# Kernel optimization log

Measured on AMD Instinct MI355X. Metric: run time of the kernel, lower is better.

## Reference

```python
import jax, jax.numpy as jnp
import numpy as np

NUM_CLASSES = 19
IGNORE = 255
KLD_MARGIN = 3.0
DEC = 0.01
BOT_EPS, TOP_EPS = 1e-4, 1.0
# eight-corner neighbor offsets (size=1), order matches AAF layers.eightcorner_activation
EDGE_OFFS = ((-1, -1), (-1, 0), (-1, 1), (0, -1), (0, 1), (1, -1), (1, 0), (1, 1))


def _shift(x, dy, dx, pad_val):
    # Shift along H,W (axes 1,2): out[:, y, x] = x[:, y+dy, x+dx], padded with pad_val.
    pads = [(0, 0), (1, 1), (1, 1)] + [(0, 0)] * (x.ndim - 3)
    xp = jnp.pad(x, pads, constant_values=pad_val)
    h, w = x.shape[1], x.shape[2]
    return xp[:, 1 + dy:1 + dy + h, 1 + dx:1 + dx + w]


def _resize_bilinear_ac(x, oh, ow):
    # torch F.interpolate(mode='bilinear', align_corners=True) on NCHW.
    n, c, h, w = x.shape
    ys = jnp.linspace(0.0, h - 1.0, oh)
    xs = jnp.linspace(0.0, w - 1.0, ow)
    y0 = jnp.floor(ys).astype(jnp.int32); y1 = jnp.minimum(y0 + 1, h - 1)
    x0 = jnp.floor(xs).astype(jnp.int32); x1 = jnp.minimum(x0 + 1, w - 1)
    wy = (ys - y0).astype(x.dtype)[None, None, :, None]
    wx = (xs - x0).astype(x.dtype)[None, None, None, :]
    rows = x[:, :, y0, :] * (1.0 - wy) + x[:, :, y1, :] * wy  # (N,C,oh,W)
    return rows[:, :, :, x0] * (1.0 - wx) + rows[:, :, :, x1] * wx  # (N,C,oh,ow)


def setup_inputs() -> dict:
    key = jax.random.key(0)
    k1, k2 = jax.random.split(key)
    preds = jax.random.normal(k1, (2, NUM_CLASSES, 64, 64), dtype=jnp.float32)
    targets = jax.random.randint(k2, (2, 512, 512), 0, NUM_CLASSES, dtype=jnp.int32)
    w_edge = jnp.zeros((1, 1, 1, NUM_CLASSES, 1, 3), dtype=jnp.float32)
    w_not_edge = jnp.zeros((1, 1, 1, NUM_CLASSES, 1, 3), dtype=jnp.float32)
    return {"preds": preds, "targets": targets, "w_edge": w_edge, "w_not_edge": w_not_edge}


def reference(preds, targets, w_edge, w_not_edge):
    h, w = targets.shape[1], targets.shape[2]
    pred = _resize_bilinear_ac(preds, h, w)          # (N,C,H,W)
    prob = jax.nn.softmax(pred, axis=1)
    prob = jnp.transpose(prob, (0, 2, 3, 1))          # (N,H,W,C) NHWC layout used by AAF layers

    labels = targets                                  # (N,H,W)
    ign = labels == IGNORE
    one_label = jnp.where(ign, 0, labels)
    ohl = jax.nn.one_hot(one_label, NUM_CLASSES, dtype=jnp.float32)  # (N,H,W,C)
    ohl = jnp.where(ign[..., None], float(IGNORE), ohl)

    # edge/non-edge class weights: softmax over last dim, take index 0 -> (1,1,1,C,1)
    w_e = jax.nn.softmax(w_edge, axis=-1)[..., 0]
    w_ne = jax.nn.softmax(w_not_edge, axis=-1)[..., 0]

    # ignores_from_label: bidirectional ignore mask, neighbor order is reversed offsets
    ignore_c = labels > NUM_CLASSES - 1               # (N,H,W)
    ignore8 = jnp.stack([_shift(ignore_c, -dy, -dx, True) | ignore_c for dy, dx in EDGE_OFFS], axis=-1)
    not_ignore = ~ignore8[:, :, :, None, :]           # (N,H,W,1,8)

    # edges_from_label: neighbor label (padded with ignore_class) differs from center
    edge8 = jnp.stack([_shift(ohl, dy, dx, float(IGNORE)) != ohl for dy, dx in EDGE_OFFS], axis=-1)  # (N,H,W,C,8)
    edge = edge8 & not_ignore
    not_edge = (~edge) & not_ignore

    # eightcorner_activation on probabilities (zero padded)
    probs_paired = jnp.stack([_shift(prob, dy, dx, 0.0) for dy, dx in EDGE_OFFS], axis=-1)  # (N,H,W,C,8)
    p = prob[..., None]                               # (N,H,W,C,1)
    pc = jnp.clip(p, BOT_EPS, TOP_EPS)
    npc = jnp.clip(1.0 - p, BOT_EPS, TOP_EPS)
    ppc = jnp.clip(probs_paired, BOT_EPS, TOP_EPS)
    nppc = jnp.clip(1.0 - probs_paired, BOT_EPS, TOP_EPS)

    # binary KL divergence per class/neighbor
    kldiv = ppc * jnp.log(ppc / pc) + nppc * jnp.log(nppc / npc)  # (N,H,W,C,8)

    # per-pixel class weights: sum_c w[c]*one_hot[c] -> (N,H,W,1,1)
    we_map = jnp.sum(w_e * ohl[..., None], axis=3, keepdims=True)
    wne_map = jnp.sum(w_ne * ohl[..., None], axis=3, keepdims=True)

    edge_loss = jnp.maximum(0.0, KLD_MARGIN - kldiv) * we_map
    not_edge_loss = kldiv * wne_map

    # torch.mean over gathered nonzero indices == masked sum / count
    e_cnt = jnp.maximum(jnp.sum(edge), 1).astype(jnp.float32)
    ne_cnt = jnp.maximum(jnp.sum(not_edge), 1).astype(jnp.float32)
    e_mean = jnp.sum(jnp.where(edge, edge_loss, 0.0)) / e_cnt
    ne_mean = jnp.sum(jnp.where(not_edge, not_edge_loss, 0.0)) / ne_cnt

    return e_mean * 1.0 * DEC + ne_mean * 1.0 * DEC
```

## Files before the change

### kernel.cpp

```cpp
#include <hip/hip_runtime.h>
#include <stdint.h>


#define NC 19
#define HH 512
#define WW 512
#define NB 2
#define TS 16
#define HS 18
#define HP (HS * HS)
#define ATRS 20
#define PS 25
#define NBLK 2048
#define LOG2E 1.4426950408889634f
#define LN2 0.6931471805599453f
#define LOG2EPS -13.287712379549449f
#define K2F 4.3280851226668906f
#define K2PAD 4.328125f

typedef _Float16 f16x2 __attribute__((ext_vector_type(2)));

#if __has_builtin(__builtin_amdgcn_exp2f)
#define EXP2F(x) __builtin_amdgcn_exp2f(x)
#else
#define EXP2F(x) __expf((x) * LN2)
#endif

#if __has_builtin(__builtin_amdgcn_fdot2)
#define FDOT2(a, b, c) __builtin_amdgcn_fdot2((a), (b), (c), false)
#else
#define FDOT2(a, b, c) fmaf((float)(a)[1], (float)(b)[1], fmaf((float)(a)[0], (float)(b)[0], (c)))
#endif

struct Part { float es, ns; unsigned int cnt, pad; };

union U32F2 { uint32_t u; f16x2 h; };
__device__ __forceinline__ uint32_t bc_u32(f16x2 v) { U32F2 x; x.h = v; return x.u; }
__device__ __forceinline__ f16x2 bc_h2(uint32_t v) { U32F2 x; x.u = v; return x.h; }
__device__ __forceinline__ float extf(f16x2 v, int h) { return h ? (float)v[1] : (float)v[0]; }

template <bool KEEP>
__device__ __forceinline__ int pix_compute(const float* __restrict__ patch,
                                           const int* __restrict__ tg,
                                           int y, int x, int y0b, int x0b,
                                           uint32_t* __restrict__ ATrow,
                                           f16x2* Dh, f16x2* Lh) {
    const bool oob = ((unsigned)y >= (unsigned)HH) | ((unsigned)x >= (unsigned)WW);
    if (oob) {
        const _Float16 aP = (_Float16)1e-4f, dP = (_Float16)LOG2EPS;
        const _Float16 tP = (_Float16)((float)aP * (float)dP);
        const uint32_t aPP = bc_u32((f16x2){aP, aP});
        const uint32_t tPP = bc_u32((f16x2){tP, tP});
        const uint32_t aPL = bc_u32((f16x2){aP, (_Float16)0.0f});
        const uint32_t tPL = bc_u32((f16x2){tP, (_Float16)0.0f});
#pragma unroll
        for (int i = 0; i < 5; ++i) {
            uint4 wv;
            wv.x = aPP; wv.y = tPP;
            wv.z = (i < 4) ? aPP : aPL;
            wv.w = (i < 4) ? tPP : tPL;
            *reinterpret_cast<uint4*>(ATrow + 4 * i) = wv;
            if (KEEP) {
                Dh[2 * i] = (f16x2){dP, dP};
                Dh[2 * i + 1] = (i < 4) ? (f16x2){dP, dP} : (f16x2){dP, (_Float16)0.0f};
                Lh[2 * i] = (f16x2){(_Float16)0.0f, (_Float16)0.0f};
                Lh[2 * i + 1] = (f16x2){(_Float16)0.0f, (_Float16)0.0f};
            }
        }
        return 255;
    }

    const int lab = tg[(y << 9) + x];
    const float fy = (float)(y * 63) / 511.0f;
    const float fx = (float)(x * 63) / 511.0f;
    const int y0 = (int)fy, x0 = (int)fx;
    const float wy = fy - (float)y0, wx = fx - (float)x0;
    const int y1 = min(y0 + 1, 63), x1 = min(x0 + 1, 63);
    const float omwy = 1.0f - wy, omwx = 1.0f - wx;
    const float w00 = omwy * omwx, w01 = omwy * wx;
    const float w10 = wy * omwx,   w11 = wy * wx;
    const int o00 = (y0 - y0b) * 5 + (x0 - x0b);
    const int o01 = o00 + (x1 - x0);
    const int o10 = o00 + (y1 - y0) * 5;
    const int o11 = o10 + (x1 - x0);

    float v2[NC], w[NC];
    float s = 0.0f;
#pragma unroll
    for (int c = 0; c < NC; ++c) {
        const float* pc_ = &patch[c * PS];
        const float vv = fmaf(pc_[o00], w00, fmaf(pc_[o01], w01,
                          fmaf(pc_[o10], w10, pc_[o11] * w11)));
        v2[c] = vv;
        const float e = EXP2F(vv);
        w[c] = e;
        s += e;
    }
    const float inv = 1.0f / s;
    const float lns2 = __log2f(s);

#pragma unroll
    for (int i = 0; i < 5; ++i) {
        _Float16 av[4], tv[4], dv[4], lv[4];
#pragma unroll
        for (int q = 0; q < 4; ++q) {
            const int c = 4 * i + q;
            _Float16 a16 = (_Float16)0.0f, d16 = (_Float16)0.0f,
                     l16 = (_Float16)0.0f, t16 = (_Float16)0.0f;
            if (c < NC) {
                const float p = w[c] * inv;
                const float la = fmaxf(v2[c] - lns2, LOG2EPS);
                const float aa = fmaxf(p, 1e-4f);
                const float lb = __log2f(fmaxf(1.0f - p, 1e-4f));
                a16 = (_Float16)aa;
                d16 = (_Float16)(la - lb);
                l16 = (_Float16)lb;
                t16 = a16 * d16 + l16;
            }
            av[q] = a16; tv[q] = t16; dv[q] = d16; lv[q] = l16;
        }
        uint4 wv;
        wv.x = bc_u32((f16x2){av[0], av[1]});
        wv.y = bc_u32((f16x2){tv[0], tv[1]});
        wv.z = bc_u32((f16x2){av[2], av[3]});
        wv.w = bc_u32((f16x2){tv[2], tv[3]});
        *reinterpret_cast<uint4*>(ATrow + 4 * i) = wv;
        if (KEEP) {
            Dh[2 * i] = (f16x2){dv[0], dv[1]};
            Dh[2 * i + 1] = (f16x2){dv[2], dv[3]};
            Lh[2 * i] = (f16x2){lv[0], lv[1]};
            Lh[2 * i + 1] = (f16x2){lv[2], lv[3]};
        }
    }
    return lab;
}

__global__ __launch_bounds__(256, 5) void k_fused(const float* __restrict__ preds,
                                                  const int* __restrict__ targets,
                                                  const float* __restrict__ w_edge,
                                                  const float* __restrict__ w_not_edge,
                                                  Part* __restrict__ pb) {
    __shared__ __align__(16) uint32_t AT[HP * ATRS];
    __shared__ int   TG[HP];
    __shared__ float swe[NC], swn[NC];
    __shared__ float patch[NC * PS];
    __shared__ float r_es[4], r_ns[4];
    __shared__ unsigned int r_cnt[4];

    const int tid = threadIdx.x;
    const int bx = blockIdx.x, by = blockIdx.y, n = blockIdx.z;

    if (tid < NC) {
        {
            float a = w_edge[tid * 3 + 0], b = w_edge[tid * 3 + 1], c = w_edge[tid * 3 + 2];
            float m = fmaxf(a, fmaxf(b, c));
            float ea = __expf(a - m), eb = __expf(b - m), ec = __expf(c - m);
            swe[tid] = (ea / (ea + eb + ec)) * LN2;
        }
        {
            float a = w_not_edge[tid * 3 + 0], b = w_not_edge[tid * 3 + 1], c = w_not_edge[tid * 3 + 2];
            float m = fmaxf(a, fmaxf(b, c));
            float ea = __expf(a - m), eb = __expf(b - m), ec = __expf(c - m);
            swn[tid] = (ea / (ea + eb + ec)) * LN2;
        }
    }

    const int* tg = targets + (n << 18);
    const float* pbase = preds + (size_t)n * NC * 4096;

    const int ty = tid >> 4, tx = tid & 15;
    const int hi = (ty + 1) * HS + (tx + 1);
    const int DOFF[8] = {-HS - 1, -HS, -HS + 1, -1, 1, HS - 1, HS, HS + 1};
    const f16x2 one2 = {(_Float16)1.0f, (_Float16)1.0f};
    const f16x2 k32 = {(_Float16)K2F, (_Float16)K2F};
    const f16x2 z2 = {(_Float16)0.0f, (_Float16)0.0f};

    float e_s = 0.0f, ne_s = 0.0f;
    unsigned int cnt = 0;

    const int yT = max(by * TS - 1, 0), xL = max(bx * TS - 1, 0);
    const int y0b = (yT * 63) / 511, x0b = (xL * 63) / 511;
    for (int t = tid; t < NC * PS; t += 256) {
        const int c = t / PS, r = t - c * PS;
        const int ry = r / 5, rx = r - ry * 5;
        const int sy = min(y0b + ry, 63), sx = min(x0b + rx, 63);
        patch[t] = pbase[c * 4096 + (sy << 6) + sx] * LOG2E;
    }
    __syncthreads();

    if (tid < 68) {
        int i;
        if (tid < 18)      i = tid;
        else if (tid < 36) i = 306 + (tid - 18);
        else if (tid < 52) i = (tid - 35) * HS;
        else               i = (tid - 51) * HS + 17;
        const int hy = i / HS, hx = i - hy * HS;
        TG[i] = pix_compute<false>(patch, tg, by * TS + hy - 1, bx * TS + hx - 1,
                                   y0b, x0b, &AT[i * ATRS], nullptr, nullptr);
    }

    f16x2 Dh[10], Lh[10];
    const int lab = pix_compute<true>(patch, tg, by * TS + ty, bx * TS + tx,
                                      y0b, x0b, &AT[hi * ATRS], Dh, Lh);
    TG[hi] = lab;
    __syncthreads();

    const bool interior_blk = (bx > 0) & (bx < 31) & (by > 0) & (by < 31);
    const int plab = lab >> 1, hlab = lab & 1;
    float es_h = 0.0f, ns_h = 0.0f;
    unsigned int cnt_h = 0;

    if (interior_blk) {
#pragma unroll
        for (int k = 0; k < 8; ++k) {
            const int np = hi + DOFF[k];
            const int nlab = TG[np];
            const int pn = nlab >> 1, hn = nlab & 1;
            const uint32_t* wbp = &AT[np * ATRS];
            float dot0 = 0.0f, dot1 = 0.0f;
            f16x2 klLw = z2, klNw = z2;
#pragma unroll
            for (int i = 0; i < 5; ++i) {
                const uint4 rd = *reinterpret_cast<const uint4*>(wbp + 4 * i);
                const int j0 = 2 * i, j1 = 2 * i + 1;
                const f16x2 kl20 = bc_h2(rd.y) - (bc_h2(rd.x) * Dh[j0] + Lh[j0]);
                const f16x2 kl21 = bc_h2(rd.w) - (bc_h2(rd.z) * Dh[j1] + Lh[j1]);
                dot0 = FDOT2(kl20, one2, dot0);
                dot1 = FDOT2(kl21, one2, dot1);
                klLw = (j0 == plab) ? kl20 : klLw;
                klLw = (j1 == plab) ? kl21 : klLw;
                klNw = (j0 == pn) ? kl20 : klNw;
                klNw = (j1 == pn) ? kl21 : klNw;
            }
            const float dot = dot0 + dot1;
            const float klL = extf(klLw, hlab);
            const float klN = extf(klNw, hn);
            const bool df = (lab != nlab);
            const float w = df ? 1.0f : 0.0f;
            es_h = fmaf(w, fmaxf(K2F - klL, 0.0f) + fmaxf(K2F - klN, 0.0f), es_h);
            ns_h += dot - w * (klL + klN);
            cnt_h += df ? ((2u << 16) | (NC - 2)) : NC;
        }
        e_s = fmaf(es_h, swe[lab], e_s);
        ne_s = fmaf(ns_h, swn[lab], ne_s);
        cnt += cnt_h;
    } else if (lab <= NC - 1) {
#pragma unroll
        for (int k = 0; k < 8; ++k) {
            const int off = DOFF[k];
            const int rlab = TG[hi - off];
            const int np = hi + off;
            const int nlab = TG[np];
            const int pn = nlab >> 1, hn = nlab & 1;
            const uint32_t* wbp = &AT[np * ATRS];
            float dot0 = 0.0f, dot1 = 0.0f, ekall = 0.0f;
            f16x2 klLw = z2, klNw = z2;
#pragma unroll
            for (int i = 0; i < 5; ++i) {
                const uint4 rd = *reinterpret_cast<const uint4*>(wbp + 4 * i);
                const int j0 = 2 * i, j1 = 2 * i + 1;
                const f16x2 kl20 = bc_h2(rd.y) - (bc_h2(rd.x) * Dh[j0] + Lh[j0]);
                const f16x2 kl21 = bc_h2(rd.w) - (bc_h2(rd.z) * Dh[j1] + Lh[j1]);
                dot0 = FDOT2(kl20, one2, dot0);
                dot1 = FDOT2(kl21, one2, dot1);
                f16x2 m0 = k32 - kl20, m1 = k32 - kl21;
                m0[0] = m0[0] > (_Float16)0.0f ? m0[0] : (_Float16)0.0f;
                m0[1] = m0[1] > (_Float16)0.0f ? m0[1] : (_Float16)0.0f;
                m1[0] = m1[0] > (_Float16)0.0f ? m1[0] : (_Float16)0.0f;
                m1[1] = m1[1] > (_Float16)0.0f ? m1[1] : (_Float16)0.0f;
                ekall = FDOT2(m0, one2, ekall);
                ekall = FDOT2(m1, one2, ekall);
                klLw = (j0 == plab) ? kl20 : klLw;
                klLw = (j1 == plab) ? kl21 : klLw;
                klNw = (j0 == pn) ? kl20 : klNw;
                klNw = (j1 == pn) ? kl21 : klNw;
            }
            const float dot = dot0 + dot1;
            const float klL = extf(klLw, hlab);
            const float klN = extf(klNw, hn);
            const bool isPad = (nlab == 255);
            const bool df = (lab != nlab) && !isPad;
            const float w = df ? 1.0f : 0.0f;
            const float ek_int = w * (fmaxf(K2F - klL, 0.0f) + fmaxf(K2F - klN, 0.0f));
            const float nk_int = dot - w * (klL + klN);
            const float ek_pad = ekall - K2PAD;
            const float ek_k = isPad ? ek_pad : ek_int;
            const float nk_k = isPad ? 0.0f : nk_int;
            const unsigned int pc = isPad ? NC : (df ? 2u : 0u);
            const bool valid = (rlab <= NC - 1);
            const float vf = valid ? 1.0f : 0.0f;
            es_h = fmaf(vf, ek_k, es_h);
            ns_h = fmaf(vf, nk_k, ns_h);
            cnt_h += valid ? ((pc << 16) | (NC - pc)) : 0u;
        }
        e_s = fmaf(es_h, swe[lab], e_s);
        ne_s = fmaf(ns_h, swn[lab], ne_s);
        cnt += cnt_h;
    }

#pragma unroll
    for (int off = 32; off > 0; off >>= 1) {
        e_s  += __shfl_down(e_s, off, 64);
        ne_s += __shfl_down(ne_s, off, 64);
        cnt  += __shfl_down(cnt, off, 64);
    }
    const int wid = tid >> 6, lane = tid & 63;
    if (lane == 0) { r_es[wid] = e_s; r_ns[wid] = ne_s; r_cnt[wid] = cnt; }
    __syncthreads();
    if (tid == 0) {
        float tes = 0.0f, tns = 0.0f;
        unsigned int tc = 0;
#pragma unroll
        for (int w = 0; w < 4; ++w) { tes += r_es[w]; tns += r_ns[w]; tc += r_cnt[w]; }
        const int bid = (blockIdx.z * gridDim.y + blockIdx.y) * gridDim.x + blockIdx.x;
        pb[bid].es = tes; pb[bid].ns = tns; pb[bid].cnt = tc; pb[bid].pad = 0;
    }
}

__global__ __launch_bounds__(256) void k_final(const Part* __restrict__ pb,
                                               float* __restrict__ out) {
    const int tid = threadIdx.x;
    double es = 0.0, ns = 0.0;
    long long ec = 0, nc = 0;
    for (int i = tid; i < NBLK; i += 256) {
        es += (double)pb[i].es; ns += (double)pb[i].ns;
        const unsigned int c = pb[i].cnt;
        ec += (long long)(c >> 16); nc += (long long)(c & 0xFFFFu);
    }
#pragma unroll
    for (int off = 32; off > 0; off >>= 1) {
        es += __shfl_down(es, off, 64);
        ns += __shfl_down(ns, off, 64);
        ec += __shfl_down(ec, off, 64);
        nc += __shfl_down(nc, off, 64);
    }
    __shared__ double ses[4], sns[4];
    __shared__ long long sec[4], snc[4];
    const int wid = tid >> 6, lane = tid & 63;
    if (lane == 0) { ses[wid] = es; sns[wid] = ns; sec[wid] = ec; snc[wid] = nc; }
    __syncthreads();
    if (tid == 0) {
        double tes = 0.0, tns = 0.0;
        long long tec = 0, tnc = 0;
#pragma unroll
        for (int w = 0; w < 4; ++w) { tes += ses[w]; tns += sns[w]; tec += sec[w]; tnc += snc[w]; }
        double ecd = (double)tec; if (ecd < 1.0) ecd = 1.0;
        double ncd = (double)tnc; if (ncd < 1.0) ncd = 1.0;
        out[0] = (float)((tes / ecd) * 0.01 + (tns / ncd) * 0.01);
    }
}

extern "C" void kernel_launch(void* const* d_in, const int* in_sizes, int n_in,
                              void* d_out, int out_size, void* d_ws, size_t ws_size,
                              hipStream_t stream) {
    const float* preds      = (const float*)d_in[0];
    const int*   targets    = (const int*)d_in[1];
    const float* w_edge     = (const float*)d_in[2];
    const float* w_not_edge = (const float*)d_in[3];

    Part* pb = (Part*)d_ws;

    dim3 grid(WW / TS, HH / TS, NB);
    k_fused<<<grid, 256, 0, stream>>>(preds, targets, w_edge, w_not_edge, pb);
    k_final<<<1, 256, 0, stream>>>(pb, (float*)d_out);
}
```

Before: 88.74 us.

## Use taller 32x16 tiles with 512-thread blocks to cut halo overhead

Doubles the tile height to 32 rows with 512 threads per block, so the halo ring is recomputed for a smaller share of pixels and half as many blocks write partials. The label tile moves to bytes and the per-block counts are split into separate edge and not-edge fields to avoid 16-bit packing overflow with more pixels. In exchange, shared memory per block and register pressure under the new launch bounds rise, which may reduce occupancy. The patch size grows to 35 values per class, apparently to cover the taller source footprint.

```diff
diff --git a/kernel.cpp b/kernel.cpp
--- a/kernel.cpp
+++ b/kernel.cpp
@@ -6,12 +6,14 @@
 #define HH 512
 #define WW 512
 #define NB 2
-#define TS 16
+#define TSY 32
+#define TSX 16
 #define HS 18
-#define HP (HS * HS)
+#define VS 34
+#define HP (VS * HS)
 #define ATRS 20
-#define PS 25
-#define NBLK 2048
+#define PS 35
+#define NBLK 1024
 #define LOG2E 1.4426950408889634f
 #define LN2 0.6931471805599453f
 #define LOG2EPS -13.287712379549449f
@@ -32,7 +34,7 @@
 #define FDOT2(a, b, c) fmaf((float)(a)[1], (float)(b)[1], fmaf((float)(a)[0], (float)(b)[0], (c)))
 #endif
 
-struct Part { float es, ns; unsigned int cnt, pad; };
+struct Part { float es, ns; unsigned int ec, nc; };
 
 union U32F2 { uint32_t u; f16x2 h; };
 __device__ __forceinline__ uint32_t bc_u32(f16x2 v) { U32F2 x; x.h = v; return x.u; }
@@ -135,17 +137,17 @@
     return lab;
 }
 
-__global__ __launch_bounds__(256, 5) void k_fused(const float* __restrict__ preds,
+__global__ __launch_bounds__(512, 6) void k_fused(const float* __restrict__ preds,
                                                   const int* __restrict__ targets,
                                                   const float* __restrict__ w_edge,
                                                   const float* __restrict__ w_not_edge,
                                                   Part* __restrict__ pb) {
     __shared__ __align__(16) uint32_t AT[HP * ATRS];
-    __shared__ int   TG[HP];
+    __shared__ uint8_t TG[HP];
     __shared__ float swe[NC], swn[NC];
     __shared__ float patch[NC * PS];
-    __shared__ float r_es[4], r_ns[4];
-    __shared__ unsigned int r_cnt[4];
+    __shared__ float r_es[8], r_ns[8];
+    __shared__ unsigned int r_cnt[8];
 
     const int tid = threadIdx.x;
     const int bx = blockIdx.x, by = blockIdx.y, n = blockIdx.z;
@@ -178,9 +180,9 @@
     float e_s = 0.0f, ne_s = 0.0f;
     unsigned int cnt = 0;
 
-    const int yT = max(by * TS - 1, 0), xL = max(bx * TS - 1, 0);
+    const int yT = max(by * TSY - 1, 0), xL = max(bx * TSX - 1, 0);
     const int y0b = (yT * 63) / 511, x0b = (xL * 63) / 511;
-    for (int t = tid; t < NC * PS; t += 256) {
+    for (int t = tid; t < NC * PS; t += 512) {
         const int c = t / PS, r = t - c * PS;
         const int ry = r / 5, rx = r - ry * 5;
         const int sy = min(y0b + ry, 63), sx = min(x0b + rx, 63);
@@ -188,24 +190,24 @@
     }
     __syncthreads();
 
-    if (tid < 68) {
+    if (tid < 100) {
         int i;
         if (tid < 18)      i = tid;
-        else if (tid < 36) i = 306 + (tid - 18);
-        else if (tid < 52) i = (tid - 35) * HS;
-        else               i = (tid - 51) * HS + 17;
+        else if (tid < 36) i = 33 * HS + (tid - 18);
+        else if (tid < 68) i = (tid - 35) * HS;
+        else               i = (tid - 67) * HS + 17;
         const int hy = i / HS, hx = i - hy * HS;
-        TG[i] = pix_compute<false>(patch, tg, by * TS + hy - 1, bx * TS + hx - 1,
-                                   y0b, x0b, &AT[i * ATRS], nullptr, nullptr);
+        TG[i] = (uint8_t)pix_compute<false>(patch, tg, by * TSY + hy - 1, bx * TSX + hx - 1,
+                                            y0b, x0b, &AT[i * ATRS], nullptr, nullptr);
     }
 
     f16x2 Dh[10], Lh[10];
-    const int lab = pix_compute<true>(patch, tg, by * TS + ty, bx * TS + tx,
+    const int lab = pix_compute<true>(patch, tg, by * TSY + ty, bx * TSX + tx,
                                       y0b, x0b, &AT[hi * ATRS], Dh, Lh);
-    TG[hi] = lab;
+    TG[hi] = (uint8_t)lab;
     __syncthreads();
 
-    const bool interior_blk = (bx > 0) & (bx < 31) & (by > 0) & (by < 31);
+    const bool interior_blk = (bx > 0) & (bx < 31) & (by > 0) & (by < 15);
     const int plab = lab >> 1, hlab = lab & 1;
     float es_h = 0.0f, ns_h = 0.0f;
     unsigned int cnt_h = 0;
@@ -214,7 +216,7 @@
 #pragma unroll
         for (int k = 0; k < 8; ++k) {
             const int np = hi + DOFF[k];
-            const int nlab = TG[np];
+            const int nlab = (int)TG[np];
             const int pn = nlab >> 1, hn = nlab & 1;
             const uint32_t* wbp = &AT[np * ATRS];
             float dot0 = 0.0f, dot1 = 0.0f;
@@ -248,9 +250,9 @@
 #pragma unroll
         for (int k = 0; k < 8; ++k) {
             const int off = DOFF[k];
-            const int rlab = TG[hi - off];
+            const int rlab = (int)TG[hi - off];
             const int np = hi + off;
-            const int nlab = TG[np];
+            const int nlab = (int)TG[np];
             const int pn = nlab >> 1, hn = nlab & 1;
             const uint32_t* wbp = &AT[np * ATRS];
             float dot0 = 0.0f, dot1 = 0.0f, ekall = 0.0f;
@@ -309,11 +311,14 @@
     __syncthreads();
     if (tid == 0) {
         float tes = 0.0f, tns = 0.0f;
-        unsigned int tc = 0;
-#pragma unroll
-        for (int w = 0; w < 4; ++w) { tes += r_es[w]; tns += r_ns[w]; tc += r_cnt[w]; }
+        unsigned int tec = 0, tnc = 0;
+#pragma unroll
+        for (int w = 0; w < 8; ++w) {
+            tes += r_es[w]; tns += r_ns[w];
+            tec += r_cnt[w] >> 16; tnc += r_cnt[w] & 0xFFFFu;
+        }
         const int bid = (blockIdx.z * gridDim.y + blockIdx.y) * gridDim.x + blockIdx.x;
-        pb[bid].es = tes; pb[bid].ns = tns; pb[bid].cnt = tc; pb[bid].pad = 0;
+        pb[bid].es = tes; pb[bid].ns = tns; pb[bid].ec = tec; pb[bid].nc = tnc;
     }
 }
 
@@ -324,8 +329,7 @@
     long long ec = 0, nc = 0;
     for (int i = tid; i < NBLK; i += 256) {
         es += (double)pb[i].es; ns += (double)pb[i].ns;
-        const unsigned int c = pb[i].cnt;
-        ec += (long long)(c >> 16); nc += (long long)(c & 0xFFFFu);
+        ec += (long long)pb[i].ec; nc += (long long)pb[i].nc;
     }
 #pragma unroll
     for (int off = 32; off > 0; off >>= 1) {
@@ -360,7 +364,7 @@
 
     Part* pb = (Part*)d_ws;
 
-    dim3 grid(WW / TS, HH / TS, NB);
-    k_fused<<<grid, 256, 0, stream>>>(preds, targets, w_edge, w_not_edge, pb);
+    dim3 grid(WW / TSX, HH / TSY, NB);
+    k_fused<<<grid, 512, 0, stream>>>(preds, targets, w_edge, w_not_edge, pb);
     k_final<<<1, 256, 0, stream>>>(pb, (float*)d_out);
 }
```

New measurement: 86.32 us (median of 2 runs). 2.7% less time.

## Algebraically reduce per-neighbor KL sums to dot products with precomputed pixel terms

Applied to the files above, without the earlier changes.

Rewrites the per-neighbor binary KL summation so that the sum over classes is a single packed fp16 dot product of the neighbor's clipped probabilities against the pixel's log-ratio vector, plus precomputed per-pixel scalars (T, SL). The label and class weight of each pixel are packed together into one shared word. Per-pixel label-specific terms are computed once. In deep interior blocks, the neighbor-label KL contribution is attributed symmetrically from the owning pixel's side, which avoids extra gathers. This cuts fp16 arithmetic per neighbor and restructures the LDS layout, at the cost of more code paths, extra log2 calls and changed rounding behaviour.

```diff
diff --git a/kernel.cpp b/kernel.cpp
--- a/kernel.cpp
+++ b/kernel.cpp
@@ -33,39 +33,55 @@
 #endif
 
 struct Part { float es, ns; unsigned int cnt, pad; };
+struct Own { float SL, u, v, dlab, llab; };
 
 union U32F2 { uint32_t u; f16x2 h; };
 __device__ __forceinline__ uint32_t bc_u32(f16x2 v) { U32F2 x; x.h = v; return x.u; }
 __device__ __forceinline__ f16x2 bc_h2(uint32_t v) { U32F2 x; x.u = v; return x.h; }
 __device__ __forceinline__ float extf(f16x2 v, int h) { return h ? (float)v[1] : (float)v[0]; }
+
+union U16H { uint16_t u; _Float16 h; };
+__device__ __forceinline__ uint32_t pack_TL(int lab, float T) {
+    U16H t; t.h = (_Float16)T;
+    return ((uint32_t)lab << 16) | (uint32_t)t.u;
+}
+__device__ __forceinline__ float TL_T(uint32_t tl) {
+    U16H t; t.u = (uint16_t)(tl & 0xFFFFu);
+    return (float)t.h;
+}
 
 template <bool KEEP>
 __device__ __forceinline__ int pix_compute(const float* __restrict__ patch,
                                            const int* __restrict__ tg,
                                            int y, int x, int y0b, int x0b,
                                            uint32_t* __restrict__ ATrow,
-                                           f16x2* Dh, f16x2* Lh) {
+                                           uint32_t* __restrict__ TLw,
+                                           f16x2* Dh, f16x2* Lh, Own* os) {
     const bool oob = ((unsigned)y >= (unsigned)HH) | ((unsigned)x >= (unsigned)WW);
     if (oob) {
-        const _Float16 aP = (_Float16)1e-4f, dP = (_Float16)LOG2EPS;
-        const _Float16 tP = (_Float16)((float)aP * (float)dP);
+        const _Float16 aP = (_Float16)1e-4f;
         const uint32_t aPP = bc_u32((f16x2){aP, aP});
-        const uint32_t tPP = bc_u32((f16x2){tP, tP});
         const uint32_t aPL = bc_u32((f16x2){aP, (_Float16)0.0f});
-        const uint32_t tPL = bc_u32((f16x2){tP, (_Float16)0.0f});
-#pragma unroll
-        for (int i = 0; i < 5; ++i) {
-            uint4 wv;
-            wv.x = aPP; wv.y = tPP;
-            wv.z = (i < 4) ? aPP : aPL;
-            wv.w = (i < 4) ? tPP : tPL;
-            *reinterpret_cast<uint4*>(ATrow + 4 * i) = wv;
-            if (KEEP) {
-                Dh[2 * i] = (f16x2){dP, dP};
-                Dh[2 * i + 1] = (i < 4) ? (f16x2){dP, dP} : (f16x2){dP, (_Float16)0.0f};
-                Lh[2 * i] = (f16x2){(_Float16)0.0f, (_Float16)0.0f};
-                Lh[2 * i + 1] = (f16x2){(_Float16)0.0f, (_Float16)0.0f};
+        uint4 W0, W1, W2, W3, W4;
+        W0.x = aPP; W0.y = aPP; W0.z = aPP; W0.w = aPP;
+        W1 = W0;
+        W2.x = aPP; W2.y = aPL; W2.z = 0u; W2.w = 0u;
+        W3.x = 0u; W3.y = 0u; W3.z = 0u; W3.w = 0u;
+        W4 = W3;
+        *reinterpret_cast<uint4*>(ATrow + 0)  = W0;
+        *reinterpret_cast<uint4*>(ATrow + 4)  = W1;
+        *reinterpret_cast<uint4*>(ATrow + 8)  = W2;
+        *reinterpret_cast<uint4*>(ATrow + 12) = W3;
+        *reinterpret_cast<uint4*>(ATrow + 16) = W4;
+        *TLw = pack_TL(255, 0.0f);
+        if (KEEP) {
+            const _Float16 dP = (_Float16)LOG2EPS;
+#pragma unroll
+            for (int j = 0; j < 10; ++j) {
+                Dh[j] = (j < 9) ? (f16x2){dP, dP} : (f16x2){dP, (_Float16)0.0f};
+                Lh[j] = (f16x2){(_Float16)0.0f, (_Float16)0.0f};
             }
+            os->SL = 0.0f; os->u = 0.0f; os->v = 0.0f; os->dlab = 0.0f; os->llab = 0.0f;
         }
         return 255;
     }
@@ -99,38 +115,65 @@
     const float inv = 1.0f / s;
     const float lns2 = __log2f(s);
 
-#pragma unroll
-    for (int i = 0; i < 5; ++i) {
-        _Float16 av[4], tv[4], dv[4], lv[4];
-#pragma unroll
-        for (int q = 0; q < 4; ++q) {
-            const int c = 4 * i + q;
-            _Float16 a16 = (_Float16)0.0f, d16 = (_Float16)0.0f,
-                     l16 = (_Float16)0.0f, t16 = (_Float16)0.0f;
-            if (c < NC) {
-                const float p = w[c] * inv;
-                const float la = fmaxf(v2[c] - lns2, LOG2EPS);
-                const float aa = fmaxf(p, 1e-4f);
-                const float lb = __log2f(fmaxf(1.0f - p, 1e-4f));
-                a16 = (_Float16)aa;
-                d16 = (_Float16)(la - lb);
-                l16 = (_Float16)lb;
-                t16 = a16 * d16 + l16;
-            }
-            av[q] = a16; tv[q] = t16; dv[q] = d16; lv[q] = l16;
-        }
-        uint4 wv;
-        wv.x = bc_u32((f16x2){av[0], av[1]});
-        wv.y = bc_u32((f16x2){tv[0], tv[1]});
-        wv.z = bc_u32((f16x2){av[2], av[3]});
-        wv.w = bc_u32((f16x2){tv[2], tv[3]});
-        *reinterpret_cast<uint4*>(ATrow + 4 * i) = wv;
-        if (KEEP) {
-            Dh[2 * i] = (f16x2){dv[0], dv[1]};
-            Dh[2 * i + 1] = (f16x2){dv[2], dv[3]};
-            Lh[2 * i] = (f16x2){lv[0], lv[1]};
-            Lh[2 * i + 1] = (f16x2){lv[2], lv[3]};
-        }
+    float Tdd = 0.0f, SL = 0.0f;
+    uint32_t aw_[10], lw_[10];
+#pragma unroll
+    for (int j = 0; j < 10; ++j) {
+        _Float16 a0 = (_Float16)0.0f, l0 = (_Float16)0.0f, d0 = (_Float16)0.0f;
+        _Float16 a1 = (_Float16)0.0f, l1 = (_Float16)0.0f, d1 = (_Float16)0.0f;
+        {
+            const int c = 2 * j;
+            const float p = w[c] * inv;
+            const float la = fmaxf(v2[c] - lns2, LOG2EPS);
+            const float aa = fmaxf(p, 1e-4f);
+            const float lb = __log2f(fmaxf(1.0f - p, 1e-4f));
+            const float dd = la - lb;
+            Tdd = fmaf(aa, dd, Tdd); SL += lb;
+            a0 = (_Float16)aa; l0 = (_Float16)lb; d0 = (_Float16)dd;
+        }
+        if (2 * j + 1 < NC) {
+            const int c = 2 * j + 1;
+            const float p = w[c] * inv;
+            const float la = fmaxf(v2[c] - lns2, LOG2EPS);
+            const float aa = fmaxf(p, 1e-4f);
+            const float lb = __log2f(fmaxf(1.0f - p, 1e-4f));
+            const float dd = la - lb;
+            Tdd = fmaf(aa, dd, Tdd); SL += lb;
+            a1 = (_Float16)aa; l1 = (_Float16)lb; d1 = (_Float16)dd;
+        }
+        aw_[j] = bc_u32((f16x2){a0, a1});
+        lw_[j] = bc_u32((f16x2){l0, l1});
+        if (KEEP) { Dh[j] = (f16x2){d0, d1}; Lh[j] = (f16x2){l0, l1}; }
+    }
+    {
+        uint4 W0, W1, W2, W3, W4;
+        W0.x = aw_[0]; W0.y = aw_[1]; W0.z = aw_[2]; W0.w = aw_[3];
+        W1.x = aw_[4]; W1.y = aw_[5]; W1.z = aw_[6]; W1.w = aw_[7];
+        W2.x = aw_[8]; W2.y = aw_[9]; W2.z = lw_[0]; W2.w = lw_[1];
+        W3.x = lw_[2]; W3.y = lw_[3]; W3.z = lw_[4]; W3.w = lw_[5];
+        W4.x = lw_[6]; W4.y = lw_[7]; W4.z = lw_[8]; W4.w = lw_[9];
+        *reinterpret_cast<uint4*>(ATrow + 0)  = W0;
+        *reinterpret_cast<uint4*>(ATrow + 4)  = W1;
+        *reinterpret_cast<uint4*>(ATrow + 8)  = W2;
+        *reinterpret_cast<uint4*>(ATrow + 12) = W3;
+        *reinterpret_cast<uint4*>(ATrow + 16) = W4;
+    }
+    *TLw = pack_TL(lab, Tdd + SL);
+
+    if (KEEP) {
+        const float* pl = &patch[lab * PS];
+        const float vlab = fmaf(pl[o00], w00, fmaf(pl[o01], w01,
+                            fmaf(pl[o10], w10, pl[o11] * w11)));
+        const float p = EXP2F(vlab) * inv;
+        const float la = fmaxf(vlab - lns2, LOG2EPS);
+        const float aa = fmaxf(p, 1e-4f);
+        const float lb = __log2f(fmaxf(1.0f - p, 1e-4f));
+        const float dd = la - lb;
+        os->SL = SL;
+        os->dlab = dd;
+        os->llab = lb;
+        os->u = fmaf(aa, dd, lb);
+        os->v = aa;
     }
     return lab;
 }
@@ -141,8 +184,8 @@
                                                   const float* __restrict__ w_not_edge,
                                                   Part* __restrict__ pb) {
     __shared__ __align__(16) uint32_t AT[HP * ATRS];
-    __shared__ int   TG[HP];
-    __shared__ float swe[NC], swn[NC];
+    __shared__ uint32_t TL[HP];
+    __shared__ float2 swen[NC];
     __shared__ float patch[NC * PS];
     __shared__ float r_es[4], r_ns[4];
     __shared__ unsigned int r_cnt[4];
@@ -151,18 +194,20 @@
     const int bx = blockIdx.x, by = blockIdx.y, n = blockIdx.z;
 
     if (tid < NC) {
+        float sw_e, sw_n;
         {
             float a = w_edge[tid * 3 + 0], b = w_edge[tid * 3 + 1], c = w_edge[tid * 3 + 2];
             float m = fmaxf(a, fmaxf(b, c));
             float ea = __expf(a - m), eb = __expf(b - m), ec = __expf(c - m);
-            swe[tid] = (ea / (ea + eb + ec)) * LN2;
+            sw_e = (ea / (ea + eb + ec)) * LN2;
         }
         {
             float a = w_not_edge[tid * 3 + 0], b = w_not_edge[tid * 3 + 1], c = w_not_edge[tid * 3 + 2];
             float m = fmaxf(a, fmaxf(b, c));
             float ea = __expf(a - m), eb = __expf(b - m), ec = __expf(c - m);
-            swn[tid] = (ea / (ea + eb + ec)) * LN2;
-        }
+            sw_n = (ea / (ea + eb + ec)) * LN2;
+        }
+        swen[tid] = make_float2(sw_e, sw_n);
     }
 
     const int* tg = targets + (n << 18);
@@ -171,9 +216,10 @@
     const int ty = tid >> 4, tx = tid & 15;
     const int hi = (ty + 1) * HS + (tx + 1);
     const int DOFF[8] = {-HS - 1, -HS, -HS + 1, -1, 1, HS - 1, HS, HS + 1};
+    const int DY[8] = {-1, -1, -1, 0, 0, 1, 1, 1};
+    const int DX[8] = {-1, 0, 1, -1, 1, -1, 0, 1};
     const f16x2 one2 = {(_Float16)1.0f, (_Float16)1.0f};
     const f16x2 k32 = {(_Float16)K2F, (_Float16)K2F};
-    const f16x2 z2 = {(_Float16)0.0f, (_Float16)0.0f};
 
     float e_s = 0.0f, ne_s = 0.0f;
     unsigned int cnt = 0;
@@ -195,107 +241,192 @@
         else if (tid < 52) i = (tid - 35) * HS;
         else               i = (tid - 51) * HS + 17;
         const int hy = i / HS, hx = i - hy * HS;
-        TG[i] = pix_compute<false>(patch, tg, by * TS + hy - 1, bx * TS + hx - 1,
-                                   y0b, x0b, &AT[i * ATRS], nullptr, nullptr);
+        pix_compute<false>(patch, tg, by * TS + hy - 1, bx * TS + hx - 1,
+                           y0b, x0b, &AT[i * ATRS], &TL[i], nullptr, nullptr, nullptr);
     }
 
     f16x2 Dh[10], Lh[10];
+    Own os;
     const int lab = pix_compute<true>(patch, tg, by * TS + ty, bx * TS + tx,
-                                      y0b, x0b, &AT[hi * ATRS], Dh, Lh);
-    TG[hi] = lab;
+                                      y0b, x0b, &AT[hi * ATRS], &TL[hi], Dh, Lh, &os);
     __syncthreads();
 
     const bool interior_blk = (bx > 0) & (bx < 31) & (by > 0) & (by < 31);
+    const bool deep_blk = (bx > 1) & (bx < 30) & (by > 1) & (by < 30);
     const int plab = lab >> 1, hlab = lab & 1;
-    float es_h = 0.0f, ns_h = 0.0f;
-    unsigned int cnt_h = 0;
-
-    if (interior_blk) {
+    const float SL = os.SL, u = os.u, v = os.v, dlab = os.dlab, llab = os.llab;
+    const uint32_t* myrow = &AT[hi * ATRS];
+    float es_o = 0.0f, ns_o = 0.0f;
+    float es_w = 0.0f, ns_w = 0.0f;
+
+    if (deep_blk) {
 #pragma unroll
         for (int k = 0; k < 8; ++k) {
             const int np = hi + DOFF[k];
-            const int nlab = TG[np];
-            const int pn = nlab >> 1, hn = nlab & 1;
-            const uint32_t* wbp = &AT[np * ATRS];
-            float dot0 = 0.0f, dot1 = 0.0f;
-            f16x2 klLw = z2, klNw = z2;
-#pragma unroll
-            for (int i = 0; i < 5; ++i) {
-                const uint4 rd = *reinterpret_cast<const uint4*>(wbp + 4 * i);
-                const int j0 = 2 * i, j1 = 2 * i + 1;
-                const f16x2 kl20 = bc_h2(rd.y) - (bc_h2(rd.x) * Dh[j0] + Lh[j0]);
-                const f16x2 kl21 = bc_h2(rd.w) - (bc_h2(rd.z) * Dh[j1] + Lh[j1]);
-                dot0 = FDOT2(kl20, one2, dot0);
-                dot1 = FDOT2(kl21, one2, dot1);
-                klLw = (j0 == plab) ? kl20 : klLw;
-                klLw = (j1 == plab) ? kl21 : klLw;
-                klNw = (j0 == pn) ? kl20 : klNw;
-                klNw = (j1 == pn) ? kl21 : klNw;
+            const uint32_t tl = TL[np];
+            const int nlab = (int)(tl >> 16);
+            const float T_N = TL_T(tl);
+            const uint32_t* rb = &AT[np * ATRS];
+            const uint4 A0 = *reinterpret_cast<const uint4*>(rb);
+            const uint4 A1 = *reinterpret_cast<const uint4*>(rb + 4);
+            const uint2 A2 = *reinterpret_cast<const uint2*>(rb + 8);
+            float acc = 0.0f;
+            acc = FDOT2(bc_h2(A0.x), Dh[0], acc);
+            acc = FDOT2(bc_h2(A0.y), Dh[1], acc);
+            acc = FDOT2(bc_h2(A0.z), Dh[2], acc);
+            acc = FDOT2(bc_h2(A0.w), Dh[3], acc);
+            acc = FDOT2(bc_h2(A1.x), Dh[4], acc);
+            acc = FDOT2(bc_h2(A1.y), Dh[5], acc);
+            acc = FDOT2(bc_h2(A1.z), Dh[6], acc);
+            acc = FDOT2(bc_h2(A1.w), Dh[7], acc);
+            acc = FDOT2(bc_h2(A2.x), Dh[8], acc);
+            acc = FDOT2(bc_h2(A2.y), Dh[9], acc);
+            const float dot = T_N - acc - SL;
+            const float aN = extf(bc_h2(rb[plab]), hlab);
+            const float lN = extf(bc_h2(rb[10 + plab]), hlab);
+            const float dN = __log2f(aN) - lN;
+            const float klL = fmaf(aN, dN, lN) - fmaf(aN, dlab, llab);
+            const float klR = u - fmaf(v, dN, lN);
+            const bool df = (lab != nlab);
+            const float wg = df ? 1.0f : 0.0f;
+            const float2 sw = swen[nlab];
+            es_o = fmaf(wg, fmaxf(K2F - klL, 0.0f), es_o);
+            ns_o += dot - wg * klL;
+            es_w = fmaf(wg * sw.x, fmaxf(K2F - klR, 0.0f), es_w);
+            ns_w = fmaf(-wg * sw.y, klR, ns_w);
+            cnt += df ? ((2u << 16) | (NC - 2)) : NC;
+        }
+    } else if (interior_blk) {
+        const int gy = by * TS + ty, gx = bx * TS + tx;
+#pragma unroll
+        for (int k = 0; k < 8; ++k) {
+            const int np = hi + DOFF[k];
+            const uint32_t tl = TL[np];
+            const int nlab = (int)(tl >> 16);
+            const float T_N = TL_T(tl);
+            const uint32_t* rb = &AT[np * ATRS];
+            const uint4 A0 = *reinterpret_cast<const uint4*>(rb);
+            const uint4 A1 = *reinterpret_cast<const uint4*>(rb + 4);
+            const uint2 A2 = *reinterpret_cast<const uint2*>(rb + 8);
+            float acc = 0.0f;
+            acc = FDOT2(bc_h2(A0.x), Dh[0], acc);
+            acc = FDOT2(bc_h2(A0.y), Dh[1], acc);
+            acc = FDOT2(bc_h2(A0.z), Dh[2], acc);
+            acc = FDOT2(bc_h2(A0.w), Dh[3], acc);
+            acc = FDOT2(bc_h2(A1.x), Dh[4], acc);
+            acc = FDOT2(bc_h2(A1.y), Dh[5], acc);
+            acc = FDOT2(bc_h2(A1.z), Dh[6], acc);
+            acc = FDOT2(bc_h2(A1.w), Dh[7], acc);
+            acc = FDOT2(bc_h2(A2.x), Dh[8], acc);
+            acc = FDOT2(bc_h2(A2.y), Dh[9], acc);
+            const float dot = T_N - acc - SL;
+            const float aN = extf(bc_h2(rb[plab]), hlab);
+            const float lN = extf(bc_h2(rb[10 + plab]), hlab);
+            const float dN = __log2f(aN) - lN;
+            const float klL = fmaf(aN, dN, lN) - fmaf(aN, dlab, llab);
+            const bool df = (lab != nlab);
+            const float wg = df ? 1.0f : 0.0f;
+            const int gyN = gy + DY[k], gxN = gx + DX[k];
+            const bool E = ((unsigned)(gyN - 16) < 480u) & ((unsigned)(gxN - 16) < 480u);
+            if (E) {
+                const float klR = u - fmaf(v, dN, lN);
+                const float2 sw = swen[nlab];
+                es_o = fmaf(wg, fmaxf(K2F - klL, 0.0f), es_o);
+                ns_o += dot - wg * klL;
+                es_w = fmaf(wg * sw.x, fmaxf(K2F - klR, 0.0f), es_w);
+                ns_w = fmaf(-wg * sw.y, klR, ns_w);
+            } else {
+                const int pn = nlab >> 1, hn = nlab & 1;
+                const float aN2 = extf(bc_h2(rb[pn]), hn);
+                const float lN2 = extf(bc_h2(rb[10 + pn]), hn);
+                const float dN2 = __log2f(aN2) - lN2;
+                const float ao = extf(bc_h2(myrow[pn]), hn);
+                const float lo = extf(bc_h2(myrow[10 + pn]), hn);
+                const float doo = __log2f(ao) - lo;
+                const float klN = fmaf(aN2, dN2, lN2) - fmaf(aN2, doo, lo);
+                es_o = fmaf(wg, fmaxf(K2F - klL, 0.0f) + fmaxf(K2F - klN, 0.0f), es_o);
+                ns_o += dot - wg * (klL + klN);
             }
-            const float dot = dot0 + dot1;
-            const float klL = extf(klLw, hlab);
-            const float klN = extf(klNw, hn);
-            const bool df = (lab != nlab);
-            const float w = df ? 1.0f : 0.0f;
-            es_h = fmaf(w, fmaxf(K2F - klL, 0.0f) + fmaxf(K2F - klN, 0.0f), es_h);
-            ns_h += dot - w * (klL + klN);
-            cnt_h += df ? ((2u << 16) | (NC - 2)) : NC;
-        }
-        e_s = fmaf(es_h, swe[lab], e_s);
-        ne_s = fmaf(ns_h, swn[lab], ne_s);
-        cnt += cnt_h;
+            cnt += df ? ((2u << 16) | (NC - 2)) : NC;
+        }
     } else if (lab <= NC - 1) {
+        const _Float16 aP = (_Float16)1e-4f, dP = (_Float16)LOG2EPS;
+        const _Float16 tP = (_Float16)((float)aP * (float)dP);
+        const f16x2 ap2 = {aP, aP}, ap2L = {aP, (_Float16)0.0f};
+        const f16x2 tp2 = {tP, tP}, tp2L = {tP, (_Float16)0.0f};
 #pragma unroll
         for (int k = 0; k < 8; ++k) {
             const int off = DOFF[k];
-            const int rlab = TG[hi - off];
+            const int rlab = (int)(TL[hi - off] >> 16);
+            const bool rvalid = (rlab <= NC - 1);
             const int np = hi + off;
-            const int nlab = TG[np];
-            const int pn = nlab >> 1, hn = nlab & 1;
-            const uint32_t* wbp = &AT[np * ATRS];
-            float dot0 = 0.0f, dot1 = 0.0f, ekall = 0.0f;
-            f16x2 klLw = z2, klNw = z2;
-#pragma unroll
-            for (int i = 0; i < 5; ++i) {
-                const uint4 rd = *reinterpret_cast<const uint4*>(wbp + 4 * i);
-                const int j0 = 2 * i, j1 = 2 * i + 1;
-                const f16x2 kl20 = bc_h2(rd.y) - (bc_h2(rd.x) * Dh[j0] + Lh[j0]);
-                const f16x2 kl21 = bc_h2(rd.w) - (bc_h2(rd.z) * Dh[j1] + Lh[j1]);
-                dot0 = FDOT2(kl20, one2, dot0);
-                dot1 = FDOT2(kl21, one2, dot1);
-                f16x2 m0 = k32 - kl20, m1 = k32 - kl21;
-                m0[0] = m0[0] > (_Float16)0.0f ? m0[0] : (_Float16)0.0f;
-                m0[1] = m0[1] > (_Float16)0.0f ? m0[1] : (_Float16)0.0f;
-                m1[0] = m1[0] > (_Float16)0.0f ? m1[0] : (_Float16)0.0f;
-                m1[1] = m1[1] > (_Float16)0.0f ? m1[1] : (_Float16)0.0f;
-                ekall = FDOT2(m0, one2, ekall);
-                ekall = FDOT2(m1, one2, ekall);
-                klLw = (j0 == plab) ? kl20 : klLw;
-                klLw = (j1 == plab) ? kl21 : klLw;
-                klNw = (j0 == pn) ? kl20 : klNw;
-                klNw = (j1 == pn) ? kl21 : klNw;
+            const uint32_t tl = TL[np];
+            const int nlab = (int)(tl >> 16);
+            const bool isPad = (nlab == 255);
+            float ek_k, nk_k;
+            unsigned int pc;
+            if (isPad) {
+                float ekall = 0.0f;
+#pragma unroll
+                for (int j = 0; j < 10; ++j) {
+                    const f16x2 a2 = (j < 9) ? ap2 : ap2L;
+                    const f16x2 t2 = (j < 9) ? tp2 : tp2L;
+                    f16x2 kl = t2 - (a2 * Dh[j] + Lh[j]);
+                    f16x2 m = k32 - kl;
+                    m[0] = m[0] > (_Float16)0.0f ? m[0] : (_Float16)0.0f;
+                    m[1] = m[1] > (_Float16)0.0f ? m[1] : (_Float16)0.0f;
+                    ekall = FDOT2(m, one2, ekall);
+                }
+                ek_k = ekall - K2PAD;
+                nk_k = 0.0f;
+                pc = NC;
+            } else {
+                const float T_N = TL_T(tl);
+                const uint32_t* rb = &AT[np * ATRS];
+                const uint4 A0 = *reinterpret_cast<const uint4*>(rb);
+                const uint4 A1 = *reinterpret_cast<const uint4*>(rb + 4);
+                const uint2 A2 = *reinterpret_cast<const uint2*>(rb + 8);
+                float acc = 0.0f;
+                acc = FDOT2(bc_h2(A0.x), Dh[0], acc);
+                acc = FDOT2(bc_h2(A0.y), Dh[1], acc);
+                acc = FDOT2(bc_h2(A0.z), Dh[2], acc);
+                acc = FDOT2(bc_h2(A0.w), Dh[3], acc);
+                acc = FDOT2(bc_h2(A1.x), Dh[4], acc);
+                acc = FDOT2(bc_h2(A1.y), Dh[5], acc);
+                acc = FDOT2(bc_h2(A1.z), Dh[6], acc);
+                acc = FDOT2(bc_h2(A1.w), Dh[7], acc);
+                acc = FDOT2(bc_h2(A2.x), Dh[8], acc);
+                acc = FDOT2(bc_h2(A2.y), Dh[9], acc);
+                const float dot = T_N - acc - SL;
+                const float aN = extf(bc_h2(rb[plab]), hlab);
+                const float lN = extf(bc_h2(rb[10 + plab]), hlab);
+                const float dN = __log2f(aN) - lN;
+                const float klL = fmaf(aN, dN, lN) - fmaf(aN, dlab, llab);
+                const int pn = nlab >> 1, hn = nlab & 1;
+                const float aN2 = extf(bc_h2(rb[pn]), hn);
+                const float lN2 = extf(bc_h2(rb[10 + pn]), hn);
+                const float dN2 = __log2f(aN2) - lN2;
+                const float ao = extf(bc_h2(myrow[pn]), hn);
+                const float lo = extf(bc_h2(myrow[10 + pn]), hn);
+                const float doo = __log2f(ao) - lo;
+                const float klN = fmaf(aN2, dN2, lN2) - fmaf(aN2, doo, lo);
+                const bool df = (lab != nlab);
+                const float wg = df ? 1.0f : 0.0f;
+                ek_k = wg * (fmaxf(K2F - klL, 0.0f) + fmaxf(K2F - klN, 0.0f));
+                nk_k = dot - wg * (klL + klN);
+                pc = df ? 2u : 0u;
             }
-            const float dot = dot0 + dot1;
-            const float klL = extf(klLw, hlab);
-            const float klN = extf(klNw, hn);
-            const bool isPad = (nlab == 255);
-            const bool df = (lab != nlab) && !isPad;
-            const float w = df ? 1.0f : 0.0f;
-            const float ek_int = w * (fmaxf(K2F - klL, 0.0f) + fmaxf(K2F - klN, 0.0f));
-            const float nk_int = dot - w * (klL + klN);
-            const float ek_pad = ekall - K2PAD;
-            const float ek_k = isPad ? ek_pad : ek_int;
-            const float nk_k = isPad ? 0.0f : nk_int;
-            const unsigned int pc = isPad ? NC : (df ? 2u : 0u);
-            const bool valid = (rlab <= NC - 1);
-            const float vf = valid ? 1.0f : 0.0f;
-            es_h = fmaf(vf, ek_k, es_h);
-            ns_h = fmaf(vf, nk_k, ns_h);
-            cnt_h += valid ? ((pc << 16) | (NC - pc)) : 0u;
-        }
-        e_s = fmaf(es_h, swe[lab], e_s);
-        ne_s = fmaf(ns_h, swn[lab], ne_s);
-        cnt += cnt_h;
+            const float vf = rvalid ? 1.0f : 0.0f;
+            es_o = fmaf(vf, ek_k, es_o);
+            ns_o = fmaf(vf, nk_k, ns_o);
+            cnt += rvalid ? ((pc << 16) | (NC - pc)) : 0u;
+        }
+    }
+
+    {
+        const float2 swl = swen[lab <= NC - 1 ? lab : 0];
+        e_s  = fmaf(es_o, swl.x, es_w);
+        ne_s = fmaf(ns_o, swl.y, ns_w);
     }
 
 #pragma unroll
```

Result: slower. 98.41 us (+10.9%).
